# Kernel optimization log

Hardware: AMD Instinct MI355X
Metric: run time of the kernel (lower is better)

The kernel has to match this reference:

```python
import jax, jax.numpy as jnp
import numpy as np

N_NODES = 16384
H = 128


def setup_inputs() -> dict:
    key = jax.random.key(0)
    k1, k2, k3, k4, k5 = jax.random.split(key, 5)
    neighbour_h = jax.random.normal(k1, (N_NODES, 2, H), dtype=jnp.float32)
    A = jax.random.uniform(k2, (H, H, 3 * H), dtype=jnp.float32)  # th.rand
    U1_w = jax.random.normal(k3, (3 * H, H), dtype=jnp.float32)   # Linear weight (out,in), no bias
    U2_w = jax.random.normal(k4, (3 * H, H), dtype=jnp.float32)
    U2_b = jax.random.normal(k5, (3 * H,), dtype=jnp.float32)
    return {"neighbour_h": neighbour_h, "A": A, "U1_w": U1_w, "U2_w": U2_w, "U2_b": U2_b}


def reference(neighbour_h, A, U1_w, U2_w, U2_b):
    # compute_iou_gate of BinaryFullTensorCell (pos_stationarity=False)
    n, _, h = neighbour_h.shape
    h1 = neighbour_h[:, 0, :]  # (n, h)
    h2 = neighbour_h[:, 1, :]  # (n, h)
    # bilinear: einsum('ijk,ni,nj->nk') -- contract via per-node outer product
    # then a single GEMM against A reshaped to (h*h, 3h).
    outer = h1[:, :, None] * h2[:, None, :]          # (n, h, h)
    bil = outer.reshape(n, h * h) @ A.reshape(h * h, -1)  # (n, 3h)
    # torch Linear: x @ W.T (+ b)
    out = bil + h1 @ U1_w.T + h2 @ U2_w.T + U2_b
    return out
```

## Files before the change

kernel.cpp:

```cpp
#include <hip/hip_runtime.h>
#include <hip/hip_bf16.h>

typedef __attribute__((ext_vector_type(8))) short bf16x8;
typedef __attribute__((ext_vector_type(16))) float f32x16;
typedef __attribute__((ext_vector_type(4))) float f32x4;
typedef __attribute__((ext_vector_type(4))) unsigned int uint4v;
typedef unsigned short ushort_t;
typedef unsigned int uint_t;

#define N_NODES 16384
#define HD 128
#define NOUT 384
#define PART_ELEMS 6291456

static __device__ __forceinline__ ushort_t f2bf(float f) {
  __hip_bfloat16 b = __float2bfloat16(f);
  return *reinterpret_cast<ushort_t*>(&b);
}

__global__ void prep_all(const float* __restrict__ A, const float* __restrict__ U1,
                         const float* __restrict__ U2, const float* __restrict__ nh,
                         ushort_t* __restrict__ pk, ushort_t* __restrict__ h1,
                         ushort_t* __restrict__ h2, float* __restrict__ h1tf) {
  __shared__ __align__(16) char smem[49152];
  const int b = blockIdx.x;
  const int t = threadIdx.x;

  if (b < 260) {
    short* spk = reinterpret_cast<short*>(smem);
    const int half = b & 1;
    const int gg = t >> 5, ll = t & 31;
    if (b < 256) {
      const int it = b >> 1;
      const size_t krow0 = (size_t)it * 128 + half * 64;
#pragma unroll 4
      for (int kl = 0; kl < 64; ++kl) {
        float v = A[(krow0 + kl) * NOUT + t];
        int cl = kl >> 4, oc = (kl >> 3) & 1, j = kl & 7;
        spk[(gg * 8 + cl * 2 + oc) * 256 + ll * 8 + j] = f2bf(v);
      }
    } else {
      const int u = (b - 256) >> 1;
      const float* U = u ? U2 : U1;
#pragma unroll 4
      for (int kl = 0; kl < 64; ++kl) {
        float v = U[(size_t)t * HD + half * 64 + kl];
        int cl = kl >> 4, oc = (kl >> 3) & 1, j = kl & 7;
        spk[(gg * 8 + cl * 2 + oc) * 256 + ll * 8 + j] = f2bf(v);
      }
    }
    __syncthreads();
    const int it_out = (b < 256) ? (b >> 1) : (128 + ((b - 256) >> 1));
    const int f = t * 64;
    const int g = f >> 11;
    const int inner = f & 2047;
    ushort_t* dst = pk + (size_t)it_out * 49152 + g * 4096 + half * 2048 + inner;
    const uint4* src = reinterpret_cast<const uint4*>(spk + f);
    uint4* d4 = reinterpret_cast<uint4*>(dst);
#pragma unroll
    for (int q = 0; q < 8; ++q) d4[q] = src[q];
  } else {
    if (t < 256) {
      float (*sm)[65] = reinterpret_cast<float(*)[65]>(smem);
      const int g = b - 260;
      const int mt = g & 255, jt = g >> 8;
      const int tx = t & 63, ty = t >> 6;
      const int m0 = mt * 64, j0 = jt * 64;
#pragma unroll
      for (int s = 0; s < 16; ++s) {
        int mm = ty + s * 4;
        float f1 = nh[(size_t)(m0 + mm) * 256 + j0 + tx];
        float f2 = nh[(size_t)(m0 + mm) * 256 + 128 + j0 + tx];
        h1[(size_t)(m0 + mm) * HD + j0 + tx] = f2bf(f1);
        h2[(size_t)(m0 + mm) * HD + j0 + tx] = f2bf(f2);
        sm[mm][tx] = f1;
      }
      __syncthreads();
#pragma unroll
      for (int s = 0; s < 16; ++s) {
        int jj = ty + s * 4;
        h1tf[(size_t)(j0 + jj) * N_NODES + m0 + tx] = sm[tx][jj];
      }
    }
  }
}

#define PK_STEP 98304
#define SLICE_B 17408

#define STAGE(IT, R)                                                              \
  do {                                                                            \
    const char* s_ = pkbase + (size_t)(IT) * PK_STEP;                             \
    char* d_ = ldsb + (R) * SLICE_B;                                              \
    __builtin_amdgcn_global_load_lds((const uint_t*)(s_ + stg),                   \
                                     (uint_t*)(d_ + wv * 1024), 16, 0, 0);        \
    __builtin_amdgcn_global_load_lds((const uint_t*)(s_ + 8192 + stg),            \
                                     (uint_t*)(d_ + 8192 + wv * 1024), 16, 0, 0); \
    const int ith_ = (IT) < 128 ? (IT) : 127;                                     \
    const char* h_ = reinterpret_cast<const char*>(                               \
                         h1tf + (size_t)ith_ * N_NODES + Mt * 256) + wv * 128;    \
    if (lane < 8)                                                                 \
      __builtin_amdgcn_global_load_lds((const uint_t*)(h_ + lane * 16),           \
                                       (uint_t*)(d_ + 16384 + wv * 128), 16, 0, 0); \
  } while (0)

__global__ __launch_bounds__(512, 2)
void gemm_kernel(const ushort_t* __restrict__ pk, const ushort_t* __restrict__ h1bf,
                 const ushort_t* __restrict__ h2bf, const float* __restrict__ h1tf,
                 const float* __restrict__ u2b, float* __restrict__ part) {
  __shared__ __align__(16) char ldsb[3 * SLICE_B];

  const int tid = threadIdx.x;
  const int bid = blockIdx.x;
  const int v  = (bid & 7) * 96 + (bid >> 3);
  const int Mt = v & 63;
  const int q  = v >> 6;
  const int Nt = q >> 1;
  const int ks = q & 1;

  const int lane = tid & 63, wv = tid >> 6;
  const int l31 = lane & 31, oct = lane >> 5;
  const int wm = wv >> 1, wn = wv & 1;
  const int mbase = Mt * 256 + wm * 64;
  const int n0w = Nt * 64 + wn * 32;
  const int g0 = Nt * 2;

  uint4v h2u[2][8];
#pragma unroll
  for (int ms = 0; ms < 2; ++ms) {
    const ushort_t* hp = h2bf + (size_t)(mbase + ms * 32 + l31) * HD + oct * 8;
#pragma unroll
    for (int c = 0; c < 8; ++c)
      h2u[ms][c] = *reinterpret_cast<const uint4v*>(hp + c * 16);
  }

  f32x16 acc[2];
  if (ks) {
#pragma unroll
    for (int qq = 0; qq < 4; ++qq) {
      f32x4 bq = *reinterpret_cast<const f32x4*>(u2b + n0w + 8 * qq + 4 * oct);
#pragma unroll
      for (int j = 0; j < 4; ++j) { acc[0][qq * 4 + j] = bq[j]; acc[1][qq * 4 + j] = bq[j]; }
    }
  } else {
    acc[0] = (f32x16)(0.0f);
    acc[1] = (f32x16)(0.0f);
  }

  const int it0 = ks ? 65 : 0;
  const int it1 = ks ? 128 : 65;

  const char* pkbase = reinterpret_cast<const char*>(pk) + (size_t)g0 * 8192;
  const int stg = wv * 1024 + lane * 16;

  const f32x16 vz = (f32x16)(0.0f);

  STAGE(it0, 0);
  STAGE(it0 + 1, 1);
  asm volatile("s_waitcnt vmcnt(3)" ::: "memory");
  __builtin_amdgcn_s_barrier();

  int r = 0, rs = 2;
  for (int it = it0; it < it1; ++it) {
    STAGE(it + 2, rs);

    const char* lb = ldsb + r * SLICE_B;
    const float s0 = *reinterpret_cast<const float*>(lb + 16384 + (wm * 64 + l31) * 4);
    const float s1 = *reinterpret_cast<const float*>(lb + 16384 + (wm * 64 + 32 + l31) * 4);

    const char* bbase = lb + wn * 8192 + oct * 512 + l31 * 16;
    uint4v bb[8];
#pragma unroll
    for (int c = 0; c < 8; ++c)
      bb[c] = *reinterpret_cast<const uint4v*>(bbase + c * 1024);

    f32x16 P0 = vz, P1 = vz;
    __builtin_amdgcn_s_setprio(1);
#pragma unroll
    for (int c = 0; c < 8; ++c) {
      bf16x8 bfr = __builtin_bit_cast(bf16x8, bb[c]);
      P0 = __builtin_amdgcn_mfma_f32_32x32x16_bf16(
          bfr, __builtin_bit_cast(bf16x8, h2u[0][c]), P0, 0, 0, 0);
      P1 = __builtin_amdgcn_mfma_f32_32x32x16_bf16(
          bfr, __builtin_bit_cast(bf16x8, h2u[1][c]), P1, 0, 0, 0);
    }
    __builtin_amdgcn_s_setprio(0);
#pragma unroll
    for (int rr = 0; rr < 16; ++rr) {
      acc[0][rr] += s0 * P0[rr];
      acc[1][rr] += s1 * P1[rr];
    }

    asm volatile("s_waitcnt vmcnt(3)" ::: "memory");
    __builtin_amdgcn_s_barrier();
    r = (r == 2) ? 0 : r + 1;
    rs = (rs == 2) ? 0 : rs + 1;
  }

  if (ks) {
    const char* bt = reinterpret_cast<const char*>(pk) +
                     (size_t)128 * PK_STEP + (size_t)((g0 + wn) * 16 + oct) * 512 +
                     (size_t)l31 * 16;
#pragma unroll
    for (int c = 0; c < 8; ++c) {
      bf16x8 bfr = __builtin_bit_cast(bf16x8, *reinterpret_cast<const uint4v*>(bt + c * 1024));
#pragma unroll
      for (int ms = 0; ms < 2; ++ms) {
        bf16x8 a = *reinterpret_cast<const bf16x8*>(
            h1bf + (size_t)(mbase + ms * 32 + l31) * HD + c * 16 + oct * 8);
        acc[ms] = __builtin_amdgcn_mfma_f32_32x32x16_bf16(bfr, a, acc[ms], 0, 0, 0);
      }
    }
    const char* bt2 = bt + PK_STEP;
#pragma unroll
    for (int c = 0; c < 8; ++c) {
      bf16x8 bfr = __builtin_bit_cast(bf16x8, *reinterpret_cast<const uint4v*>(bt2 + c * 1024));
#pragma unroll
      for (int ms = 0; ms < 2; ++ms) {
        acc[ms] = __builtin_amdgcn_mfma_f32_32x32x16_bf16(
            bfr, __builtin_bit_cast(bf16x8, h2u[ms][c]), acc[ms], 0, 0, 0);
      }
    }
  }

  float* my = part + (size_t)ks * PART_ELEMS;
#pragma unroll
  for (int ms = 0; ms < 2; ++ms) {
    float* rowp = my + (size_t)(mbase + ms * 32 + l31) * NOUT + n0w + 4 * oct;
#pragma unroll
    for (int qq = 0; qq < 4; ++qq) {
      f32x4 o;
      o[0] = acc[ms][qq * 4 + 0];
      o[1] = acc[ms][qq * 4 + 1];
      o[2] = acc[ms][qq * 4 + 2];
      o[3] = acc[ms][qq * 4 + 3];
      *reinterpret_cast<f32x4*>(rowp + 8 * qq) = o;
    }
  }
}

__global__ void reduce2(const float* __restrict__ part, float* __restrict__ out) {
  int i = blockIdx.x * 256 + threadIdx.x;
  float4 a = reinterpret_cast<const float4*>(part)[i];
  float4 b = reinterpret_cast<const float4*>(part + PART_ELEMS)[i];
  float4 o;
  o.x = a.x + b.x; o.y = a.y + b.y; o.z = a.z + b.z; o.w = a.w + b.w;
  reinterpret_cast<float4*>(out)[i] = o;
}

extern "C" void kernel_launch(void* const* d_in, const int* in_sizes, int n_in,
                              void* d_out, int out_size, void* d_ws, size_t ws_size,
                              hipStream_t stream) {
  const float* nh  = (const float*)d_in[0];
  const float* A   = (const float*)d_in[1];
  const float* U1  = (const float*)d_in[2];
  const float* U2  = (const float*)d_in[3];
  const float* U2b = (const float*)d_in[4];

  char* ws = (char*)d_ws;
  ushort_t* pk   = (ushort_t*)(ws);
  ushort_t* h1bf = (ushort_t*)(ws + 12779520);
  ushort_t* h2bf = (ushort_t*)(ws + 16973824);
  float*    h1tf = (float*)(ws + 21168128);
  float*    part = (float*)(ws + 29556736);

  prep_all<<<dim3(772), 384, 0, stream>>>(A, U1, U2, nh, pk, h1bf, h2bf, h1tf);
  gemm_kernel<<<dim3(768), 512, 0, stream>>>(pk, h1bf, h2bf, h1tf, U2b, part);
  reduce2<<<dim3(6144), 256, 0, stream>>>(part, (float*)d_out);
}
```

Measured before the change: 308.7 us.

## Software-pipeline bilinear GEMM loop with double-buffered LDS fragments and deferred scaling

Unrolls the main k-loop by two and double-buffers the register fragments read from LDS. The next slice's B fragments and h1 scalars are read right after the barrier, while the current slice's MFMA chain runs. The scaled accumulate of the previous slice's partial products is also deferred so it overlaps the MFMA chain. This is meant to hide LDS read latency and the VALU tail behind the matrix cores, at the cost of more live registers and a possible spill under the 2-blocks-per-CU launch bound.

```diff
diff --git a/kernel.cpp b/kernel.cpp
--- a/kernel.cpp
+++ b/kernel.cpp
@@ -104,6 +104,41 @@
                                        (uint_t*)(d_ + 16384 + wv * 128), 16, 0, 0); \
   } while (0)
 
+#define READ_NEXT(BBN, SN0, SN1, RN)                                              \
+  do {                                                                            \
+    const char* lb_ = ldsb + (RN) * SLICE_B;                                      \
+    const char* bb_ = lb_ + wn * 8192 + oct * 512 + l31 * 16;                     \
+    _Pragma("unroll")                                                             \
+    for (int c = 0; c < 8; ++c)                                                   \
+      BBN[c] = *reinterpret_cast<const uint4v*>(bb_ + c * 1024);                  \
+    SN0 = *reinterpret_cast<const float*>(lb_ + 16384 + (wm * 64 + l31) * 4);     \
+    SN1 = *reinterpret_cast<const float*>(lb_ + 16384 + (wm * 64 + 32 + l31) * 4);\
+  } while (0)
+
+#define CHAIN(BBC, PC0, PC1)                                                      \
+  do {                                                                            \
+    PC0 = vz; PC1 = vz;                                                           \
+    __builtin_amdgcn_s_setprio(1);                                                \
+    _Pragma("unroll")                                                             \
+    for (int c = 0; c < 8; ++c) {                                                 \
+      bf16x8 f_ = __builtin_bit_cast(bf16x8, BBC[c]);                             \
+      PC0 = __builtin_amdgcn_mfma_f32_32x32x16_bf16(                              \
+          f_, __builtin_bit_cast(bf16x8, h2u[0][c]), PC0, 0, 0, 0);               \
+      PC1 = __builtin_amdgcn_mfma_f32_32x32x16_bf16(                              \
+          f_, __builtin_bit_cast(bf16x8, h2u[1][c]), PC1, 0, 0, 0);               \
+    }                                                                             \
+    __builtin_amdgcn_s_setprio(0);                                                \
+  } while (0)
+
+#define TAIL(S0_, S1_, PP0, PP1)                                                  \
+  do {                                                                            \
+    _Pragma("unroll")                                                             \
+    for (int rr = 0; rr < 16; ++rr) {                                             \
+      acc[0][rr] += (S0_) * PP0[rr];                                              \
+      acc[1][rr] += (S1_) * PP1[rr];                                              \
+    }                                                                             \
+  } while (0)
+
 __global__ __launch_bounds__(512, 2)
 void gemm_kernel(const ushort_t* __restrict__ pk, const ushort_t* __restrict__ h1bf,
                  const ushort_t* __restrict__ h2bf, const float* __restrict__ h1tf,
@@ -159,42 +194,39 @@
   STAGE(it0 + 1, 1);
   asm volatile("s_waitcnt vmcnt(3)" ::: "memory");
   __builtin_amdgcn_s_barrier();
-
-  int r = 0, rs = 2;
-  for (int it = it0; it < it1; ++it) {
-    STAGE(it + 2, rs);
-
-    const char* lb = ldsb + r * SLICE_B;
-    const float s0 = *reinterpret_cast<const float*>(lb + 16384 + (wm * 64 + l31) * 4);
-    const float s1 = *reinterpret_cast<const float*>(lb + 16384 + (wm * 64 + 32 + l31) * 4);
-
-    const char* bbase = lb + wn * 8192 + oct * 512 + l31 * 16;
-    uint4v bb[8];
-#pragma unroll
-    for (int c = 0; c < 8; ++c)
-      bb[c] = *reinterpret_cast<const uint4v*>(bbase + c * 1024);
-
-    f32x16 P0 = vz, P1 = vz;
-    __builtin_amdgcn_s_setprio(1);
-#pragma unroll
-    for (int c = 0; c < 8; ++c) {
-      bf16x8 bfr = __builtin_bit_cast(bf16x8, bb[c]);
-      P0 = __builtin_amdgcn_mfma_f32_32x32x16_bf16(
-          bfr, __builtin_bit_cast(bf16x8, h2u[0][c]), P0, 0, 0, 0);
-      P1 = __builtin_amdgcn_mfma_f32_32x32x16_bf16(
-          bfr, __builtin_bit_cast(bf16x8, h2u[1][c]), P1, 0, 0, 0);
-    }
-    __builtin_amdgcn_s_setprio(0);
-#pragma unroll
-    for (int rr = 0; rr < 16; ++rr) {
-      acc[0][rr] += s0 * P0[rr];
-      acc[1][rr] += s1 * P1[rr];
-    }
-
+  uint4v bbX[8], bbY[8];
+  f32x16 pX0, pX1, pY0 = vz, pY1 = vz;
+  float sX0, sX1, sY0 = 0.0f, sY1 = 0.0f;
+  READ_NEXT(bbX, sX0, sX1, 0);
+
+  int rn = 1, rsb = 2;
+  for (int it = it0; it < it1 - 1; it += 2) {
+    {
+      const float t0 = sY0, t1 = sY1;
+      STAGE(it + 2, rsb); rsb = (rsb == 2) ? 0 : rsb + 1;
+      asm volatile("s_waitcnt vmcnt(3)" ::: "memory");
+      __builtin_amdgcn_s_barrier();
+      READ_NEXT(bbY, sY0, sY1, rn); rn = (rn == 2) ? 0 : rn + 1;
+      TAIL(t0, t1, pY0, pY1);
+      CHAIN(bbX, pX0, pX1);
+    }
+    {
+      const float t0 = sX0, t1 = sX1;
+      STAGE(it + 3, rsb); rsb = (rsb == 2) ? 0 : rsb + 1;
+      asm volatile("s_waitcnt vmcnt(3)" ::: "memory");
+      __builtin_amdgcn_s_barrier();
+      READ_NEXT(bbX, sX0, sX1, rn); rn = (rn == 2) ? 0 : rn + 1;
+      TAIL(t0, t1, pX0, pX1);
+      CHAIN(bbY, pY0, pY1);
+    }
+  }
+  {
+    STAGE(it1 + 1, rsb);
     asm volatile("s_waitcnt vmcnt(3)" ::: "memory");
     __builtin_amdgcn_s_barrier();
-    r = (r == 2) ? 0 : r + 1;
-    rs = (rs == 2) ? 0 : rs + 1;
+    TAIL(sY0, sY1, pY0, pY1);
+    CHAIN(bbX, pX0, pX1);
+    TAIL(sX0, sX1, pX0, pX1);
   }
 
   if (ks) {
```

Result: faster. 292.2 us (-5.4%).
